# Kernel tuning notes

Measured on AMD Instinct MI355X. Metric: run time of the kernel, lower is better.

## Reference

```python
import jax, jax.numpy as jnp
import numpy as np

N, E, D, H, ED = 10000, 160000, 512, 256, 16
EPS = 1e-5  # BatchNorm1d eps


def _cgconv(x, src, dst, edge_attr, Wf, bf, Ws, bs, gamma, beta, mean, var):
    # PyG CGConv: z = [x_i, x_j, e_ij]; m = sigmoid(lin_f(z)) * softplus(lin_s(z));
    # aggr='add' at target i; batch_norm (eval mode, running stats) then residual.
    z = jnp.concatenate([x[dst], x[src], edge_attr], axis=1)  # [E, 2D+ED]
    m = jax.nn.sigmoid(z @ Wf + bf) * jax.nn.softplus(z @ Ws + bs)  # [E, D]
    aggr = jax.ops.segment_sum(m, dst, num_segments=x.shape[0])  # [N, D]
    bn = (aggr - mean) * jax.lax.rsqrt(var + EPS) * gamma + beta
    return x + bn


def _gcnconv(x, src, dst, W, b):
    # PyG GCNConv with add_self_loops=True, normalize=True:
    n = x.shape[0]
    deg = jax.ops.segment_sum(jnp.ones((src.shape[0],), x.dtype), dst, num_segments=n) + 1.0
    dinv = jax.lax.rsqrt(deg)  # [N]
    h = x @ W  # [N, out]
    out = jax.ops.segment_sum((dinv[src] * dinv[dst])[:, None] * h[src], dst, num_segments=n)
    out = out + (dinv * dinv)[:, None] * h  # self-loop contribution
    return out + b


def _forward(x, edge_attr, goal_feat,
             cg1_Wf, cg1_bf, cg1_Ws, cg1_bs, cg1_gamma, cg1_beta, cg1_mean, cg1_var,
             cg2_Wf, cg2_bf, cg2_Ws, cg2_bs, cg2_gamma, cg2_beta, cg2_mean, cg2_var,
             gcn3_W, gcn3_b, gcn4_W, gcn4_b, d1_W, d1_b, d2_W, d2_b, src, dst):
    # dropout layers are identity in eval mode (self.training=False)
    x = jax.nn.relu(_cgconv(x, src, dst, edge_attr, cg1_Wf, cg1_bf, cg1_Ws, cg1_bs,
                            cg1_gamma, cg1_beta, cg1_mean, cg1_var))
    x = jax.nn.relu(_cgconv(x, src, dst, edge_attr, cg2_Wf, cg2_bf, cg2_Ws, cg2_bs,
                            cg2_gamma, cg2_beta, cg2_mean, cg2_var))
    x = jax.nn.relu(_gcnconv(x, src, dst, gcn3_W, gcn3_b))
    x = jax.nn.relu(_gcnconv(x, src, dst, gcn4_W, gcn4_b))
    g = jnp.broadcast_to(goal_feat, (x.shape[0], goal_feat.shape[1]))  # repeat(num_nodes, 1)
    h = jax.nn.relu(jnp.concatenate([x, g], axis=1) @ d1_W + d1_b)
    return h @ d2_W + d2_b  # [N, 1]


def setup_inputs() -> dict:
    ks = jax.random.split(jax.random.key(0), 12)
    w = lambda k, s: jax.random.normal(k, s, dtype=jnp.float32) * 0.02
    Z = 2 * D + ED
    return {
        "x": jax.random.normal(ks[0], (N, D), jnp.float32),
        "edge_attr": jax.random.normal(ks[1], (E, ED), jnp.float32),
        "goal_feat": jax.random.normal(ks[2], (1, D), jnp.float32),
        "cg1_Wf": w(ks[3], (Z, D)), "cg1_bf": jnp.zeros((D,), jnp.float32),
        "cg1_Ws": w(ks[4], (Z, D)), "cg1_bs": jnp.zeros((D,), jnp.float32),
        "cg1_gamma": jnp.ones((D,), jnp.float32), "cg1_beta": jnp.zeros((D,), jnp.float32),
        "cg1_mean": jnp.zeros((D,), jnp.float32), "cg1_var": jnp.ones((D,), jnp.float32),
        "cg2_Wf": w(ks[5], (Z, D)), "cg2_bf": jnp.zeros((D,), jnp.float32),
        "cg2_Ws": w(ks[6], (Z, D)), "cg2_bs": jnp.zeros((D,), jnp.float32),
        "cg2_gamma": jnp.ones((D,), jnp.float32), "cg2_beta": jnp.zeros((D,), jnp.float32),
        "cg2_mean": jnp.zeros((D,), jnp.float32), "cg2_var": jnp.ones((D,), jnp.float32),
        "gcn3_W": w(ks[7], (D, H)), "gcn3_b": jnp.zeros((H,), jnp.float32),
        "gcn4_W": w(ks[8], (H, H)), "gcn4_b": jnp.zeros((H,), jnp.float32),
        "d1_W": w(ks[9], (H + D, D)), "d1_b": jnp.zeros((D,), jnp.float32),
        "d2_W": w(ks[10], (D, 1)), "d2_b": jnp.zeros((1,), jnp.float32),
        "edge_index": jax.random.randint(ks[11], (2, E), 0, N, dtype=jnp.int32),
        "batch": jnp.zeros((N,), jnp.int32),
    }


def reference(x, edge_attr, goal_feat,
              cg1_Wf, cg1_bf, cg1_Ws, cg1_bs, cg1_gamma, cg1_beta, cg1_mean, cg1_var,
              cg2_Wf, cg2_bf, cg2_Ws, cg2_bs, cg2_gamma, cg2_beta, cg2_mean, cg2_var,
              gcn3_W, gcn3_b, gcn4_W, gcn4_b, d1_W, d1_b, d2_W, d2_b,
              edge_index, batch):
    src, dst = edge_index[0], edge_index[1]
    return _forward(x, edge_attr, goal_feat,
                    cg1_Wf, cg1_bf, cg1_Ws, cg1_bs, cg1_gamma, cg1_beta, cg1_mean, cg1_var,
                    cg2_Wf, cg2_bf, cg2_Ws, cg2_bs, cg2_gamma, cg2_beta, cg2_mean, cg2_var,
                    gcn3_W, gcn3_b, gcn4_W, gcn4_b, d1_W, d1_b, d2_W, d2_b, src, dst)
```

## Files before the change

### kernel.cpp

```cpp
#include <hip/hip_runtime.h>
#include <math.h>

#define N_NODES 10000
#define N_EDGES 160000
#define DIM 512
#define HDIM 256
#define EDIM 16
#define BN_EPS 1e-5f
#define L2E 1.4426950408889634f
#define LN2 0.6931471805599453f

typedef unsigned short ushort_t;
typedef unsigned int uint_t;
typedef __attribute__((ext_vector_type(8))) short bf16x8;
typedef __attribute__((ext_vector_type(4))) float f32x4;
typedef __attribute__((ext_vector_type(2))) _Float16 half2_t;

__device__ __forceinline__ ushort_t f2bf(float x) {
    uint_t u = __float_as_uint(x);
    uint_t r = (u + 0x7FFF + ((u >> 16) & 1)) >> 16;
    return (ushort_t)r;
}
__device__ __forceinline__ float bf2f(ushort_t h) {
    return __uint_as_float(((uint_t)h) << 16);
}
__device__ __forceinline__ float bflo(uint_t u) {
    return __uint_as_float(u << 16);
}
__device__ __forceinline__ float bfhi(uint_t u) {
    return __uint_as_float(u & 0xffff0000u);
}
__device__ __forceinline__ void gld16(const void* g, void* l) {
    __builtin_amdgcn_global_load_lds(
        (const __attribute__((address_space(1))) unsigned int*)g,
        (__attribute__((address_space(3))) unsigned int*)l, 16, 0, 0);
}
__device__ __forceinline__ half2_t u2h(uint_t u) {
    return __builtin_bit_cast(half2_t, u);
}
__device__ __forceinline__ uint_t pk_f16(float a, float b) {
    return __builtin_bit_cast(uint_t, __builtin_amdgcn_cvt_pkrtz(a, b));
}
__device__ __forceinline__ float fexp2(float x) {
#if __has_builtin(__builtin_amdgcn_exp2f)
    return __builtin_amdgcn_exp2f(x);
#else
    return __expf(x * LN2);
#endif
}
__device__ __forceinline__ float flog2(float x) {
#if __has_builtin(__builtin_amdgcn_logf)
    return __builtin_amdgcn_logf(x);
#else
    return __logf(x) * L2E;
#endif
}
__device__ __forceinline__ void swz(int lid, int gx, int gy, int& bx, int& by) {
    int per = gy * 8;
    int grp = lid / per;
    int rem = lid - grp * per;
    int gsz = min(8, gx - grp * 8);
    by = rem / gsz;
    bx = grp * 8 + (rem - by * gsz);
}

__global__ void k_hist(const int* __restrict__ dst, int* __restrict__ cnt) {
    int e = blockIdx.x * blockDim.x + threadIdx.x;
    if (e < N_EDGES) atomicAdd(&cnt[dst[e]], 1);
}

__global__ __launch_bounds__(1024) void k_scan(int* __restrict__ offs, float* __restrict__ dinv) {
    __shared__ int wsum[16];
    __shared__ int carryS;
    int t = threadIdx.x, lane = t & 63, wv = t >> 6;
    if (t == 0) carryS = 0;
    __syncthreads();
    for (int base = 0; base < N_NODES; base += 1024) {
        int idx = base + t;
        int v = (idx < N_NODES) ? offs[idx] : 0;
        if (idx < N_NODES) dinv[idx] = rsqrtf((float)v + 1.0f);
        int s = v;
#pragma unroll
        for (int off = 1; off < 64; off <<= 1) {
            int u = __shfl_up(s, off, 64);
            if (lane >= off) s += u;
        }
        if (lane == 63) wsum[wv] = s;
        __syncthreads();
        int carry = carryS;
        if (wv == 0) {
            int w = (lane < 16) ? wsum[lane] : 0;
#pragma unroll
            for (int off = 1; off < 16; off <<= 1) {
                int u = __shfl_up(w, off, 64);
                if (lane >= off) w += u;
            }
            if (lane < 16) wsum[lane] = w;
        }
        __syncthreads();
        int wbase = (wv == 0) ? 0 : wsum[wv - 1];
        if (idx < N_NODES) offs[idx] = carry + wbase + s - v;
        int total = wsum[15];
        __syncthreads();
        if (t == 0) carryS = carry + total;
        __syncthreads();
    }
    if (t == 0) offs[N_NODES] = carryS;
}

__global__ void k_scatter(const int* __restrict__ srcv, const int* __restrict__ dstv,
                          const float* __restrict__ ea,
                          const int* __restrict__ offs, const float* __restrict__ dinv,
                          int* __restrict__ cursor,
                          int* __restrict__ srcArr, float* __restrict__ dinvArr,
                          uint_t* __restrict__ eaP) {
    int e = blockIdx.x * blockDim.x + threadIdx.x;
    if (e >= N_EDGES) return;
    int d = dstv[e];
    int p = offs[d] + atomicAdd(&cursor[d], 1);
    int s = srcv[e];
    srcArr[p] = s;
    dinvArr[p] = dinv[s];
    const float* er = ea + (size_t)e * EDIM;
    uint_t pk[8];
#pragma unroll
    for (int k2 = 0; k2 < 8; k2++) pk[k2] = pk_f16(er[2 * k2], er[2 * k2 + 1]);
    uint_t* q = eaP + (size_t)p * 8;
    *(uint4*)q = *(uint4*)&pk[0];
    *(uint4*)(q + 4) = *(uint4*)&pk[4];
}

__global__ __launch_bounds__(256) void k_cvtW(
    const float* __restrict__ Wf0, const float* __restrict__ Ws0,
    const float* __restrict__ Wf1, const float* __restrict__ Ws1,
    const float* __restrict__ g3W, const float* __restrict__ g4W,
    const float* __restrict__ d1W,
    ushort_t* __restrict__ W2cg0, ushort_t* __restrict__ W2cg1,
    ushort_t* __restrict__ W2g3, ushort_t* __restrict__ W2g4,
    ushort_t* __restrict__ W2d1)
{
    __shared__ ushort_t tle[64][72];
    int b = blockIdx.x, t = threadIdx.x;
    const float* src; int ldw, kin0, cin0, ldk, cout0, kout0; ushort_t* out; float scale;
    if (b < 512) {
        int layer = b >> 8, tt = b & 255;
        int g = tt >> 6, rem = tt & 63;
        int ct = rem >> 3, kt = rem & 7;
        const float* Wf = layer ? Wf1 : Wf0;
        const float* Ws = layer ? Ws1 : Ws0;
        src = (g & 1) ? Ws : Wf;
        ldw = 512; kin0 = ((g & 2) ? 512 : 0) + kt * 64; cin0 = ct * 64;
        out = layer ? W2cg1 : W2cg0; ldk = 512;
        cout0 = g * 512 + ct * 64; kout0 = kt * 64;
        scale = L2E;
    } else if (b < 544) {
        int tt = b - 512; int ct = tt >> 3, kt = tt & 7;
        src = g3W; ldw = 256; kin0 = kt * 64; cin0 = ct * 64;
        out = W2g3; ldk = 512; cout0 = ct * 64; kout0 = kt * 64; scale = 1.f;
    } else if (b < 560) {
        int tt = b - 544; int ct = tt >> 2, kt = tt & 3;
        src = g4W; ldw = 256; kin0 = kt * 64; cin0 = ct * 64;
        out = W2g4; ldk = 256; cout0 = ct * 64; kout0 = kt * 64; scale = 1.f;
    } else {
        int tt = b - 560; int ct = tt >> 2, kt = tt & 3;
        src = d1W; ldw = 512; kin0 = kt * 64; cin0 = ct * 64;
        out = W2d1; ldk = 256; cout0 = ct * 64; kout0 = kt * 64; scale = 1.f;
    }
    int c = t & 63;
    int k4 = t >> 6;
#pragma unroll
    for (int i = 0; i < 16; i++) {
        int k = k4 * 16 + i;
        tle[k][c] = f2bf(src[(size_t)(kin0 + k) * ldw + cin0 + c] * scale);
    }
    __syncthreads();
    int cl = t >> 2, kq = t & 3;
    ushort_t tmp[16];
#pragma unroll
    for (int j = 0; j < 16; j++) tmp[j] = tle[kq * 16 + j][cl];
    ushort_t* dst = out + (size_t)(cout0 + cl) * ldk + kout0 + kq * 16;
    *(uint4*)dst = *(uint4*)&tmp[0];
    *(uint4*)(dst + 8) = *(uint4*)&tmp[8];
}

#define MP_WEP   32
#define MP_GV    40
#define MP_END   20040

__global__ __launch_bounds__(256) void k_megaprep(
    const float* __restrict__ x, const float* __restrict__ goal,
    const float* __restrict__ Wf0, const float* __restrict__ Ws0,
    const float* __restrict__ Wf1, const float* __restrict__ Ws1,
    const float* __restrict__ d1W, const float* __restrict__ d1b,
    ushort_t* __restrict__ A2, uint_t* __restrict__ WEP, float* __restrict__ cgv)
{
    int b = blockIdx.x, t = threadIdx.x;
    if (b < MP_WEP) {
        int layer = b >> 4, blk = b & 15;
        int idx = blk * 256 + t;
        int c = idx >> 3, k2 = idx & 7;
        const float* Wf = (layer ? Wf1 : Wf0) + 1024 * 512;
        const float* Ws = (layer ? Ws1 : Ws0) + 1024 * 512;
        uint_t* WEPf = WEP + layer * 8192;
        uint_t* WEPs = WEPf + 4096;
        WEPf[c * 8 + k2] = pk_f16(Wf[(2 * k2) * 512 + c] * L2E, Wf[(2 * k2 + 1) * 512 + c] * L2E);
        WEPs[c * 8 + k2] = pk_f16(Ws[(2 * k2) * 512 + c] * L2E, Ws[(2 * k2 + 1) * 512 + c] * L2E);
    } else if (b < MP_GV) {
        __shared__ float red[256];
        int bb = b - MP_WEP;
        int c = bb * 64 + (t & 63);
        int slice = t >> 6;
        float acc = 0.f;
        for (int i = 0; i < 128; i++) {
            int k = slice * 128 + i;
            acc += goal[k] * d1W[(size_t)(256 + k) * 512 + c];
        }
        red[t] = acc;
        __syncthreads();
        if (t < 128) red[t] += red[t + 128];
        __syncthreads();
        if (t < 64) cgv[c] = red[t] + red[t + 64] + d1b[c];
    } else {
        int idx = (b - MP_GV) * 256 + t;
        if (idx < N_NODES * 512) A2[idx] = f2bf(x[idx]);
    }
}

__global__ __launch_bounds__(256) void k_gemm3(
    const ushort_t* __restrict__ A2, int K, int M,
    const ushort_t* __restrict__ W2t,
    float* __restrict__ outF, ushort_t* __restrict__ outQ,
    const float* __restrict__ bias, int mode, int ldc, int gx, int gy)
{
    __shared__ ushort_t As[128 * 64];
    __shared__ ushort_t Bs[128 * 64];
    int tid = threadIdx.x;
    int lane = tid & 63, w = tid >> 6;
    int wm = w & 1, wn = w >> 1;
    int lrow = lane & 15, quad = lane >> 4;
    int bx, by;
    swz(blockIdx.x, gx, gy, bx, by);
    int row0 = bx * 128, col0 = by * 128;

    f32x4 acc[4][4] = {};

    const ushort_t* ArG[4]; ushort_t* ArL[4];
    const ushort_t* BrG[4]; ushort_t* BrL[4];
#pragma unroll
    for (int p = 0; p < 4; p++) {
        int s = tid + 256 * p;
        int r = s >> 3, k8p = s & 7;
        int k8l = k8p ^ (r & 7);
        int gra = row0 + r; if (gra >= M) gra = M - 1;
        ArG[p] = A2 + (size_t)gra * K + k8l * 8;
        ArL[p] = As + s * 8;
        BrG[p] = W2t + (size_t)(col0 + r) * K + k8l * 8;
        BrL[p] = Bs + s * 8;
    }
    const ushort_t* afp[2][4];
    const ushort_t* bfp[2][4];
#pragma unroll
    for (int sl = 0; sl < 2; sl++)
#pragma unroll
        for (int mt = 0; mt < 4; mt++) {
            int r = wm * 64 + mt * 16 + lrow;
            afp[sl][mt] = As + (r * 8 + ((sl * 4 + quad) ^ (r & 7))) * 8;
            int c = wn * 64 + mt * 16 + lrow;
            bfp[sl][mt] = Bs + (c * 8 + ((sl * 4 + quad) ^ (c & 7))) * 8;
        }

    for (int k0 = 0; k0 < K; k0 += 64) {
        __syncthreads();
#pragma unroll
        for (int p = 0; p < 4; p++) {
            gld16(ArG[p] + k0, ArL[p]);
            gld16(BrG[p] + k0, BrL[p]);
        }
        __syncthreads();
#pragma unroll
        for (int sl = 0; sl < 2; sl++) {
            bf16x8 af[4], bff[4];
#pragma unroll
            for (int i = 0; i < 4; i++) {
                af[i]  = *(const bf16x8*)afp[sl][i];
                bff[i] = *(const bf16x8*)bfp[sl][i];
            }
#pragma unroll
            for (int mt = 0; mt < 4; mt++)
#pragma unroll
                for (int nt = 0; nt < 4; nt++)
                    acc[mt][nt] = __builtin_amdgcn_mfma_f32_16x16x32_bf16(
                        af[mt], bff[nt], acc[mt][nt], 0, 0, 0);
        }
    }

#pragma unroll
    for (int mt = 0; mt < 4; mt++) {
#pragma unroll
        for (int nt = 0; nt < 4; nt++) {
            int gcol = col0 + wn * 64 + nt * 16 + lrow;
#pragma unroll
            for (int r = 0; r < 4; r++) {
                int grow = row0 + wm * 64 + mt * 16 + quad * 4 + r;
                if (grow >= M) continue;
                float v = acc[mt][nt][r];
                if (mode == 1) {
                    if (gcol < 1024) {
                        outF[(size_t)grow * 1024 + gcol] = v;
                    } else {
                        int c = gcol - 1024;
                        int grp = c >> 9, cc = c & 511;
                        int pos = (cc >> 1) * 4 + grp * 2 + (cc & 1);
                        outQ[(size_t)grow * 1024 + pos] = f2bf(v);
                    }
                } else if (mode == 2) {
                    outF[(size_t)grow * ldc + gcol] = fmaxf(v + bias[gcol], 0.f);
                } else {
                    outQ[(size_t)grow * ldc + gcol] = f2bf(v);
                }
            }
        }
    }
}

__global__ __launch_bounds__(256) void k_gemm64(
    const ushort_t* __restrict__ A2, int K, int M,
    const ushort_t* __restrict__ W2t,
    float* __restrict__ outF, ushort_t* __restrict__ outQ,
    const float* __restrict__ bias, int mode, int ldc, int gx, int gy)
{
    __shared__ ushort_t As[64 * 64];
    __shared__ ushort_t Bs[128 * 64];
    int tid = threadIdx.x;
    int lane = tid & 63, w = tid >> 6;
    int lrow = lane & 15, quad = lane >> 4;
    int bx, by;
    swz(blockIdx.x, gx, gy, bx, by);
    int row0 = bx * 64, col0 = by * 128;

    f32x4 acc[4][2] = {};

    const ushort_t* ArG[2]; ushort_t* ArL[2];
    const ushort_t* BrG[4]; ushort_t* BrL[4];
#pragma unroll
    for (int p = 0; p < 2; p++) {
        int s = tid + 256 * p;
        int r = s >> 3, k8p = s & 7;
        int k8l = k8p ^ (r & 7);
        int gra = row0 + r; if (gra >= M) gra = M - 1;
        ArG[p] = A2 + (size_t)gra * K + k8l * 8;
        ArL[p] = As + s * 8;
    }
#pragma unroll
    for (int p = 0; p < 4; p++) {
        int s = tid + 256 * p;
        int r = s >> 3, k8p = s & 7;
        int k8l = k8p ^ (r & 7);
        BrG[p] = W2t + (size_t)(col0 + r) * K + k8l * 8;
        BrL[p] = Bs + s * 8;
    }
    const ushort_t* afp[2][4];
    const ushort_t* bfp[2][2];
#pragma unroll
    for (int sl = 0; sl < 2; sl++) {
#pragma unroll
        for (int mt = 0; mt < 4; mt++) {
            int r = mt * 16 + lrow;
            afp[sl][mt] = As + (r * 8 + ((sl * 4 + quad) ^ (r & 7))) * 8;
        }
#pragma unroll
        for (int nt = 0; nt < 2; nt++) {
            int c = w * 32 + nt * 16 + lrow;
            bfp[sl][nt] = Bs + (c * 8 + ((sl * 4 + quad) ^ (c & 7))) * 8;
        }
    }

    for (int k0 = 0; k0 < K; k0 += 64) {
        __syncthreads();
        gld16(ArG[0] + k0, ArL[0]);
        gld16(ArG[1] + k0, ArL[1]);
#pragma unroll
        for (int p = 0; p < 4; p++) gld16(BrG[p] + k0, BrL[p]);
        __syncthreads();
#pragma unroll
        for (int sl = 0; sl < 2; sl++) {
            bf16x8 af[4], bff[2];
#pragma unroll
            for (int i = 0; i < 4; i++) af[i] = *(const bf16x8*)afp[sl][i];
#pragma unroll
            for (int i = 0; i < 2; i++) bff[i] = *(const bf16x8*)bfp[sl][i];
#pragma unroll
            for (int mt = 0; mt < 4; mt++)
#pragma unroll
                for (int nt = 0; nt < 2; nt++)
                    acc[mt][nt] = __builtin_amdgcn_mfma_f32_16x16x32_bf16(
                        af[mt], bff[nt], acc[mt][nt], 0, 0, 0);
        }
    }

#pragma unroll
    for (int mt = 0; mt < 4; mt++) {
#pragma unroll
        for (int nt = 0; nt < 2; nt++) {
            int gcol = col0 + w * 32 + nt * 16 + lrow;
#pragma unroll
            for (int r = 0; r < 4; r++) {
                int grow = row0 + mt * 16 + quad * 4 + r;
                if (grow >= M) continue;
                float v = acc[mt][nt][r];
                if (mode == 2) outF[(size_t)grow * ldc + gcol] = fmaxf(v + bias[gcol], 0.f);
                else outQ[(size_t)grow * ldc + gcol] = f2bf(v);
            }
        }
    }
}

__global__ __launch_bounds__(256) void k_cg_aggr(
    const float* __restrict__ xin, const float* __restrict__ P,
    const ushort_t* __restrict__ Qi,
    const uint_t* __restrict__ WEPf, const uint_t* __restrict__ WEPs,
    const float* __restrict__ bfv, const float* __restrict__ bsv,
    const float* __restrict__ gamma, const float* __restrict__ beta,
    const float* __restrict__ mean, const float* __restrict__ var,
    const int* __restrict__ offs, const int* __restrict__ srcArr,
    const uint_t* __restrict__ eaP,
    float* __restrict__ xout, ushort_t* __restrict__ A2out)
{
    int i = blockIdx.x;
    int t = threadIdx.x;
    int c0 = 2 * t;
    uint_t wfp[2][8], wsp[2][8];
    {
        const uint_t* pf8 = WEPf + c0 * 8;
        const uint_t* ps8 = WEPs + c0 * 8;
        *(uint4*)&wfp[0][0] = *(const uint4*)(pf8 + 0);
        *(uint4*)&wfp[0][4] = *(const uint4*)(pf8 + 4);
        *(uint4*)&wfp[1][0] = *(const uint4*)(pf8 + 8);
        *(uint4*)&wfp[1][4] = *(const uint4*)(pf8 + 12);
        *(uint4*)&wsp[0][0] = *(const uint4*)(ps8 + 0);
        *(uint4*)&wsp[0][4] = *(const uint4*)(ps8 + 4);
        *(uint4*)&wsp[1][0] = *(const uint4*)(ps8 + 8);
        *(uint4*)&wsp[1][4] = *(const uint4*)(ps8 + 12);
    }
    float2 pf = *(const float2*)&P[(size_t)i * 1024 + c0];
    float2 ps = *(const float2*)&P[(size_t)i * 1024 + 512 + c0];
    float2 bf2 = *(const float2*)&bfv[c0];
    float2 bs2 = *(const float2*)&bsv[c0];
    pf.x = fmaf(bf2.x, L2E, pf.x); pf.y = fmaf(bf2.y, L2E, pf.y);
    ps.x = fmaf(bs2.x, L2E, ps.x); ps.y = fmaf(bs2.y, L2E, ps.y);
    float acc0 = 0.f, acc1 = 0.f;
    int e0 = offs[i], e1 = offs[i + 1];
    __shared__ uint_t sEaP[32][8];
    __shared__ int sSrc[34];
    const ushort_t* Qbase = Qi + 4 * t;
    for (int base = e0; base < e1; base += 32) {
        int g = min(32, e1 - base);
        __syncthreads();
        if (t < 34) {
            int s = 0;
            if (t < g) s = srcArr[base + t];
            sSrc[t] = s;
        }
        {
            int j = t >> 3, k2 = t & 7;
            if (j < g) sEaP[j][k2] = eaP[(size_t)(base + j) * 8 + k2];
        }
        __syncthreads();
        uint2 q0 = *(const uint2*)(Qbase + ((size_t)sSrc[0] << 10));
        uint2 q1 = *(const uint2*)(Qbase + ((size_t)sSrc[1] << 10));
        for (int j = 0; j < g; j++) {
            uint2 qn = *(const uint2*)(Qbase + ((size_t)sSrc[j + 2] << 10));
            uint4 eA = *(const uint4*)&sEaP[j][0];
            uint4 eB = *(const uint4*)&sEaP[j][4];
            float gf0 = pf.x + bflo(q0.x), gf1 = pf.y + bfhi(q0.x);
            float gs0 = ps.x + bflo(q0.y), gs1 = ps.y + bfhi(q0.y);
            uint_t ek[8] = {eA.x, eA.y, eA.z, eA.w, eB.x, eB.y, eB.z, eB.w};
#pragma unroll
            for (int k = 0; k < 8; k++) {
                half2_t e2 = u2h(ek[k]);
                gf0 = __builtin_amdgcn_fdot2(e2, u2h(wfp[0][k]), gf0, false);
                gf1 = __builtin_amdgcn_fdot2(e2, u2h(wfp[1][k]), gf1, false);
                gs0 = __builtin_amdgcn_fdot2(e2, u2h(wsp[0][k]), gs0, false);
                gs1 = __builtin_amdgcn_fdot2(e2, u2h(wsp[1][k]), gs1, false);
            }
            float sg0 = __builtin_amdgcn_rcpf(1.f + fexp2(-gf0));
            float sg1 = __builtin_amdgcn_rcpf(1.f + fexp2(-gf1));
            float sp0 = fmaxf(gs0, 0.f) + flog2(1.f + fexp2(-fabsf(gs0)));
            float sp1 = fmaxf(gs1, 0.f) + flog2(1.f + fexp2(-fabsf(gs1)));
            acc0 = fmaf(sg0, sp0, acc0);
            acc1 = fmaf(sg1, sp1, acc1);
            q0 = q1; q1 = qn;
        }
    }
    acc0 *= LN2;
    acc1 *= LN2;
    size_t ib = (size_t)i * DIM;
    float2 mn = *(const float2*)&mean[c0];
    float2 vr = *(const float2*)&var[c0];
    float2 gm = *(const float2*)&gamma[c0];
    float2 bt = *(const float2*)&beta[c0];
    float2 xi = *(const float2*)&xin[ib + c0];
    float bn0 = (acc0 - mn.x) * rsqrtf(vr.x + BN_EPS) * gm.x + bt.x;
    float bn1 = (acc1 - mn.y) * rsqrtf(vr.y + BN_EPS) * gm.y + bt.y;
    float o0 = fmaxf(xi.x + bn0, 0.f);
    float o1 = fmaxf(xi.y + bn1, 0.f);
    if (xout) *(float2*)&xout[ib + c0] = make_float2(o0, o1);
    ushort_t h0 = f2bf(o0), h1 = f2bf(o1);
    *(uint_t*)(A2out + (size_t)i * 512 + c0) = (uint_t)h0 | ((uint_t)h1 << 16);
}

__global__ __launch_bounds__(128) void k_gcn_aggr(
    const ushort_t* __restrict__ h, const float* __restrict__ dinv,
    const float* __restrict__ bias,
    const int* __restrict__ offs, const int* __restrict__ srcArr,
    const float* __restrict__ dinvArr, ushort_t* __restrict__ A2out)
{
    int i = blockIdx.x;
    int t = threadIdx.x;
    int c0 = 2 * t;
    float acc0 = 0.f, acc1 = 0.f;
    int e0 = offs[i], e1 = offs[i + 1];
    __shared__ int sS[36];
    __shared__ float sD[36];
    for (int base = e0; base < e1; base += 32) {
        int g = min(32, e1 - base);
        __syncthreads();
        if (t < 36) {
            bool ok = (t < g);
            sS[t] = ok ? srcArr[base + t] : 0;
            sD[t] = ok ? dinvArr[base + t] : 0.f;
        }
        __syncthreads();
        uint_t q0 = *(const uint_t*)(h + (size_t)sS[0] * HDIM + c0);
        uint_t q1 = *(const uint_t*)(h + (size_t)sS[1] * HDIM + c0);
        uint_t q2 = *(const uint_t*)(h + (size_t)sS[2] * HDIM + c0);
        uint_t q3 = *(const uint_t*)(h + (size_t)sS[3] * HDIM + c0);
        for (int j = 0; j < g; j++) {
            uint_t qn = *(const uint_t*)(h + (size_t)sS[j + 4] * HDIM + c0);
            acc0 += sD[j] * bflo(q0);
            acc1 += sD[j] * bfhi(q0);
            q0 = q1; q1 = q2; q2 = q3; q3 = qn;
        }
    }
    float di = dinv[i];
    uint_t qi = *(const uint_t*)(h + (size_t)i * HDIM + c0);
    float2 b2 = *(const float2*)&bias[c0];
    float o0 = fmaxf(di * acc0 + di * di * bflo(qi) + b2.x, 0.f);
    float o1 = fmaxf(di * acc1 + di * di * bfhi(qi) + b2.y, 0.f);
    ushort_t h0 = f2bf(o0), h1 = f2bf(o1);
    *(uint_t*)(A2out + (size_t)i * 256 + c0) = (uint_t)h0 | ((uint_t)h1 << 16);
}

__global__ __launch_bounds__(256) void k_final(const float* __restrict__ hd,
                                               const float* __restrict__ w2,
                                               const float* __restrict__ b2,
                                               float* __restrict__ out) {
    int wave = threadIdx.x >> 6, lane = threadIdx.x & 63;
    int i = blockIdx.x * 4 + wave;
    if (i >= N_NODES) return;
    const float* r = hd + (size_t)i * DIM;
    float acc = 0.f;
#pragma unroll
    for (int q = 0; q < 8; q++) acc += r[lane + 64 * q] * w2[lane + 64 * q];
#pragma unroll
    for (int off = 32; off > 0; off >>= 1) acc += __shfl_down(acc, off, 64);
    if (lane == 0) out[i] = acc + b2[0];
}

extern "C" void kernel_launch(void* const* d_in, const int* in_sizes, int n_in,
                              void* d_out, int out_size, void* d_ws, size_t ws_size,
                              hipStream_t stream) {
    (void)in_sizes; (void)n_in; (void)out_size; (void)ws_size;
    const float* x      = (const float*)d_in[0];
    const float* ea     = (const float*)d_in[1];
    const float* goal   = (const float*)d_in[2];
    const float* cgWf[2] = {(const float*)d_in[3],  (const float*)d_in[11]};
    const float* cgbf[2] = {(const float*)d_in[4],  (const float*)d_in[12]};
    const float* cgWs[2] = {(const float*)d_in[5],  (const float*)d_in[13]};
    const float* cgbs[2] = {(const float*)d_in[6],  (const float*)d_in[14]};
    const float* cggm[2] = {(const float*)d_in[7],  (const float*)d_in[15]};
    const float* cgbt[2] = {(const float*)d_in[8],  (const float*)d_in[16]};
    const float* cgmn[2] = {(const float*)d_in[9],  (const float*)d_in[17]};
    const float* cgvr[2] = {(const float*)d_in[10], (const float*)d_in[18]};
    const float* gcn3_W = (const float*)d_in[19];
    const float* gcn3_b = (const float*)d_in[20];
    const float* gcn4_W = (const float*)d_in[21];
    const float* gcn4_b = (const float*)d_in[22];
    const float* d1_W   = (const float*)d_in[23];
    const float* d1_b   = (const float*)d_in[24];
    const float* d2_W   = (const float*)d_in[25];
    const float* d2_b   = (const float*)d_in[26];
    const int*   eidx   = (const int*)d_in[27];
    const int*   srcv   = eidx;
    const int*   dstv   = eidx + N_EDGES;
    float* outp = (float*)d_out;

    char* w = (char*)d_ws;
    float*    Pbuf  = (float*)w;                      w += (size_t)N_NODES * 1024 * 4;
    ushort_t* Qbuf  = (ushort_t*)w;                   w += (size_t)N_NODES * 1024 * 2;
    float*    xB    = (float*)w;                      w += (size_t)N_NODES * 512 * 4;
    ushort_t* A2    = (ushort_t*)w;                   w += (size_t)N_NODES * 512 * 2;
    ushort_t* A3    = (ushort_t*)w;                   w += (size_t)N_NODES * 256 * 2;
    ushort_t* W2cg0 = (ushort_t*)w;                   w += (size_t)2048 * 512 * 2;
    ushort_t* W2cg1 = (ushort_t*)w;                   w += (size_t)2048 * 512 * 2;
    ushort_t* W2g3  = (ushort_t*)w;                   w += (size_t)256 * 512 * 2;
    ushort_t* W2g4  = (ushort_t*)w;                   w += (size_t)256 * 256 * 2;
    ushort_t* W2d1  = (ushort_t*)w;                   w += (size_t)512 * 256 * 2;
    uint_t*   eaP   = (uint_t*)w;                     w += (size_t)N_EDGES * 8 * 4;
    uint_t*   WEP   = (uint_t*)w;                     w += 16384 * 4;
    float*    cgv   = (float*)w;                      w += 512 * 4;
    int*      srcArr  = (int*)w;                      w += N_EDGES * 4;
    float*    dinvArr = (float*)w;                    w += N_EDGES * 4;
    int*      offs    = (int*)w;                      w += (N_NODES + 1) * 4;
    int*      cursor  = (int*)w;                      w += N_NODES * 4;
    float*    dinv    = (float*)w;                    w += N_NODES * 4;
    uint_t* WEPf[2] = {WEP, WEP + 8192};
    uint_t* WEPs[2] = {WEP + 4096, WEP + 12288};
    ushort_t* h3 = (ushort_t*)Pbuf;
    float*    hd = (float*)Qbuf;

    k_cvtW<<<592, 256, 0, stream>>>(cgWf[0], cgWs[0], cgWf[1], cgWs[1],
                                    gcn3_W, gcn4_W, d1_W,
                                    W2cg0, W2cg1, W2g3, W2g4, W2d1);
    k_megaprep<<<MP_END, 256, 0, stream>>>(x, goal,
        cgWf[0], cgWs[0], cgWf[1], cgWs[1], d1_W, d1_b, A2, WEP, cgv);

    hipMemsetAsync(offs, 0, (N_NODES + 1) * sizeof(int), stream);
    hipMemsetAsync(cursor, 0, N_NODES * sizeof(int), stream);
    k_hist<<<(N_EDGES + 255) / 256, 256, 0, stream>>>(dstv, offs);
    k_scan<<<1, 1024, 0, stream>>>(offs, dinv);
    k_scatter<<<(N_EDGES + 255) / 256, 256, 0, stream>>>(srcv, dstv, ea, offs, dinv,
                                                         cursor, srcArr, dinvArr, eaP);

    k_gemm3<<<79 * 16, 256, 0, stream>>>(A2, 512, N_NODES, W2cg0,
                                         Pbuf, Qbuf, nullptr, 1, 0, 79, 16);
    k_cg_aggr<<<N_NODES, 256, 0, stream>>>(x, Pbuf, Qbuf, WEPf[0], WEPs[0],
                                           cgbf[0], cgbs[0],
                                           cggm[0], cgbt[0], cgmn[0], cgvr[0],
                                           offs, srcArr, eaP, xB, A2);
    k_gemm3<<<79 * 16, 256, 0, stream>>>(A2, 512, N_NODES, W2cg1,
                                         Pbuf, Qbuf, nullptr, 1, 0, 79, 16);
    k_cg_aggr<<<N_NODES, 256, 0, stream>>>(xB, Pbuf, Qbuf, WEPf[1], WEPs[1],
                                           cgbf[1], cgbs[1],
                                           cggm[1], cgbt[1], cgmn[1], cgvr[1],
                                           offs, srcArr, eaP, nullptr, A2);

    k_gemm64<<<157 * 2, 256, 0, stream>>>(A2, 512, N_NODES, W2g3,
                                          nullptr, h3, nullptr, 3, HDIM, 157, 2);
    k_gcn_aggr<<<N_NODES, 128, 0, stream>>>(h3, dinv, gcn3_b, offs, srcArr, dinvArr, A3);

    k_gemm64<<<157 * 2, 256, 0, stream>>>(A3, 256, N_NODES, W2g4,
                                          nullptr, h3, nullptr, 3, HDIM, 157, 2);
    k_gcn_aggr<<<N_NODES, 128, 0, stream>>>(h3, dinv, gcn4_b, offs, srcArr, dinvArr, A3);

    k_gemm64<<<157 * 4, 256, 0, stream>>>(A3, 256, N_NODES, W2d1,
                                          hd, nullptr, cgv, 2, DIM, 157, 4);
    k_final<<<(N_NODES + 3) / 4, 256, 0, stream>>>(hd, d2_W, d2_b, outp);
}
```

Before: 561.4 us.

## Deepen gather prefetch in aggregation kernels and single-pass scan

The CG and GCN aggregation loops now prefetch 4 and 8 neighbor rows ahead using a rotating register ring, with the loop unrolled to match. The scatter kernel stores source indices already scaled to byte offsets, so the gathers skip the multiply. The CSR scan becomes a single pass where each thread handles 10 nodes, replacing the serial loop over 1024-node chunks. The aim is more memory-level parallelism on the random gathers and less scan latency. The cost is extra register pressure and a second index array to write.

Measured after the change: 536.0 us. 1.05x faster.

```diff
diff --git a/kernel.cpp b/kernel.cpp
--- a/kernel.cpp
+++ b/kernel.cpp
@@ -71,55 +71,61 @@
 
 __global__ __launch_bounds__(1024) void k_scan(int* __restrict__ offs, float* __restrict__ dinv) {
     __shared__ int wsum[16];
-    __shared__ int carryS;
     int t = threadIdx.x, lane = t & 63, wv = t >> 6;
-    if (t == 0) carryS = 0;
+    int base_i = t * 10;
+    int v[10];
+    int s = 0;
+#pragma unroll
+    for (int k = 0; k < 10; k++) {
+        int idx = base_i + k;
+        int x = (idx < N_NODES) ? offs[idx] : 0;
+        v[k] = x;
+        s += x;
+        if (idx < N_NODES) dinv[idx] = rsqrtf((float)x + 1.0f);
+    }
+    int ps = s;
+#pragma unroll
+    for (int off = 1; off < 64; off <<= 1) {
+        int u = __shfl_up(ps, off, 64);
+        if (lane >= off) ps += u;
+    }
+    if (lane == 63) wsum[wv] = ps;
     __syncthreads();
-    for (int base = 0; base < N_NODES; base += 1024) {
-        int idx = base + t;
-        int v = (idx < N_NODES) ? offs[idx] : 0;
-        if (idx < N_NODES) dinv[idx] = rsqrtf((float)v + 1.0f);
-        int s = v;
-#pragma unroll
-        for (int off = 1; off < 64; off <<= 1) {
-            int u = __shfl_up(s, off, 64);
-            if (lane >= off) s += u;
-        }
-        if (lane == 63) wsum[wv] = s;
-        __syncthreads();
-        int carry = carryS;
-        if (wv == 0) {
-            int w = (lane < 16) ? wsum[lane] : 0;
-#pragma unroll
-            for (int off = 1; off < 16; off <<= 1) {
-                int u = __shfl_up(w, off, 64);
-                if (lane >= off) w += u;
-            }
-            if (lane < 16) wsum[lane] = w;
-        }
-        __syncthreads();
-        int wbase = (wv == 0) ? 0 : wsum[wv - 1];
-        if (idx < N_NODES) offs[idx] = carry + wbase + s - v;
-        int total = wsum[15];
-        __syncthreads();
-        if (t == 0) carryS = carry + total;
-        __syncthreads();
-    }
-    if (t == 0) offs[N_NODES] = carryS;
+    if (wv == 0) {
+        int w = (lane < 16) ? wsum[lane] : 0;
+#pragma unroll
+        for (int off = 1; off < 16; off <<= 1) {
+            int u = __shfl_up(w, off, 64);
+            if (lane >= off) w += u;
+        }
+        if (lane < 16) wsum[lane] = w;
+    }
+    __syncthreads();
+    int wbase = (wv == 0) ? 0 : wsum[wv - 1];
+    int run = wbase + ps - s;
+#pragma unroll
+    for (int k = 0; k < 10; k++) {
+        int idx = base_i + k;
+        if (idx < N_NODES) offs[idx] = run;
+        run += v[k];
+    }
+    if (t == 1023) offs[N_NODES] = wsum[15];
 }
 
 __global__ void k_scatter(const int* __restrict__ srcv, const int* __restrict__ dstv,
                           const float* __restrict__ ea,
                           const int* __restrict__ offs, const float* __restrict__ dinv,
                           int* __restrict__ cursor,
-                          int* __restrict__ srcArr, float* __restrict__ dinvArr,
+                          int* __restrict__ srcQ, int* __restrict__ srcH,
+                          float* __restrict__ dinvArr,
                           uint_t* __restrict__ eaP) {
     int e = blockIdx.x * blockDim.x + threadIdx.x;
     if (e >= N_EDGES) return;
     int d = dstv[e];
     int p = offs[d] + atomicAdd(&cursor[d], 1);
     int s = srcv[e];
-    srcArr[p] = s;
+    srcQ[p] = s << 11;
+    srcH[p] = s << 9;
     dinvArr[p] = dinv[s];
     const float* er = ea + (size_t)e * EDIM;
     uint_t pk[8];
@@ -415,6 +421,28 @@
     }
 }
 
+#define CG_BODY(curq, jj) do {                                                     \
+    uint4 eA = *(const uint4*)&sEaP[jj][0];                                        \
+    uint4 eB = *(const uint4*)&sEaP[jj][4];                                        \
+    float gf0 = pf.x + bflo((curq).x), gf1 = pf.y + bfhi((curq).x);                \
+    float gs0 = ps.x + bflo((curq).y), gs1 = ps.y + bfhi((curq).y);                \
+    uint_t ek[8] = {eA.x, eA.y, eA.z, eA.w, eB.x, eB.y, eB.z, eB.w};               \
+    _Pragma("unroll")                                                              \
+    for (int k = 0; k < 8; k++) {                                                  \
+        half2_t e2 = u2h(ek[k]);                                                   \
+        gf0 = __builtin_amdgcn_fdot2(e2, u2h(wfp[0][k]), gf0, false);              \
+        gf1 = __builtin_amdgcn_fdot2(e2, u2h(wfp[1][k]), gf1, false);              \
+        gs0 = __builtin_amdgcn_fdot2(e2, u2h(wsp[0][k]), gs0, false);              \
+        gs1 = __builtin_amdgcn_fdot2(e2, u2h(wsp[1][k]), gs1, false);              \
+    }                                                                              \
+    float sg0 = __builtin_amdgcn_rcpf(1.f + fexp2(-gf0));                          \
+    float sg1 = __builtin_amdgcn_rcpf(1.f + fexp2(-gf1));                          \
+    float sp0 = fmaxf(gs0, 0.f) + flog2(1.f + fexp2(-fabsf(gs0)));                 \
+    float sp1 = fmaxf(gs1, 0.f) + flog2(1.f + fexp2(-fabsf(gs1)));                 \
+    acc0 = fmaf(sg0, sp0, acc0);                                                   \
+    acc1 = fmaf(sg1, sp1, acc1);                                                   \
+} while (0)
+
 __global__ __launch_bounds__(256) void k_cg_aggr(
     const float* __restrict__ xin, const float* __restrict__ P,
     const ushort_t* __restrict__ Qi,
@@ -422,7 +450,7 @@
     const float* __restrict__ bfv, const float* __restrict__ bsv,
     const float* __restrict__ gamma, const float* __restrict__ beta,
     const float* __restrict__ mean, const float* __restrict__ var,
-    const int* __restrict__ offs, const int* __restrict__ srcArr,
+    const int* __restrict__ offs, const int* __restrict__ srcQ,
     const uint_t* __restrict__ eaP,
     float* __restrict__ xout, ushort_t* __restrict__ A2out)
 {
@@ -451,45 +479,32 @@
     float acc0 = 0.f, acc1 = 0.f;
     int e0 = offs[i], e1 = offs[i + 1];
     __shared__ uint_t sEaP[32][8];
-    __shared__ int sSrc[34];
-    const ushort_t* Qbase = Qi + 4 * t;
+    __shared__ int sOff[36];
+    const char* Qb = (const char*)(Qi + 4 * t);
     for (int base = e0; base < e1; base += 32) {
         int g = min(32, e1 - base);
         __syncthreads();
-        if (t < 34) {
-            int s = 0;
-            if (t < g) s = srcArr[base + t];
-            sSrc[t] = s;
-        }
+        if (t < 36) sOff[t] = (t < g) ? srcQ[base + t] : 0;
         {
             int j = t >> 3, k2 = t & 7;
             if (j < g) sEaP[j][k2] = eaP[(size_t)(base + j) * 8 + k2];
         }
         __syncthreads();
-        uint2 q0 = *(const uint2*)(Qbase + ((size_t)sSrc[0] << 10));
-        uint2 q1 = *(const uint2*)(Qbase + ((size_t)sSrc[1] << 10));
-        for (int j = 0; j < g; j++) {
-            uint2 qn = *(const uint2*)(Qbase + ((size_t)sSrc[j + 2] << 10));
-            uint4 eA = *(const uint4*)&sEaP[j][0];
-            uint4 eB = *(const uint4*)&sEaP[j][4];
-            float gf0 = pf.x + bflo(q0.x), gf1 = pf.y + bfhi(q0.x);
-            float gs0 = ps.x + bflo(q0.y), gs1 = ps.y + bfhi(q0.y);
-            uint_t ek[8] = {eA.x, eA.y, eA.z, eA.w, eB.x, eB.y, eB.z, eB.w};
-#pragma unroll
-            for (int k = 0; k < 8; k++) {
-                half2_t e2 = u2h(ek[k]);
-                gf0 = __builtin_amdgcn_fdot2(e2, u2h(wfp[0][k]), gf0, false);
-                gf1 = __builtin_amdgcn_fdot2(e2, u2h(wfp[1][k]), gf1, false);
-                gs0 = __builtin_amdgcn_fdot2(e2, u2h(wsp[0][k]), gs0, false);
-                gs1 = __builtin_amdgcn_fdot2(e2, u2h(wsp[1][k]), gs1, false);
+        uint2 q[4];
+#pragma unroll
+        for (int p = 0; p < 4; p++) q[p] = *(const uint2*)(Qb + (uint_t)sOff[p]);
+        int j = 0;
+        for (; j + 4 <= g; j += 4) {
+#pragma unroll
+            for (int u = 0; u < 4; u++) {
+                uint2 cur = q[u];
+                q[u] = *(const uint2*)(Qb + (uint_t)sOff[j + u + 4]);
+                CG_BODY(cur, j + u);
             }
-            float sg0 = __builtin_amdgcn_rcpf(1.f + fexp2(-gf0));
-            float sg1 = __builtin_amdgcn_rcpf(1.f + fexp2(-gf1));
-            float sp0 = fmaxf(gs0, 0.f) + flog2(1.f + fexp2(-fabsf(gs0)));
-            float sp1 = fmaxf(gs1, 0.f) + flog2(1.f + fexp2(-fabsf(gs1)));
-            acc0 = fmaf(sg0, sp0, acc0);
-            acc1 = fmaf(sg1, sp1, acc1);
-            q0 = q1; q1 = qn;
+        }
+#pragma unroll
+        for (int u = 0; u < 3; u++) {
+            if (j + u < g) CG_BODY(q[u], j + u);
         }
     }
     acc0 *= LN2;
@@ -512,7 +527,7 @@
 __global__ __launch_bounds__(128) void k_gcn_aggr(
     const ushort_t* __restrict__ h, const float* __restrict__ dinv,
     const float* __restrict__ bias,
-    const int* __restrict__ offs, const int* __restrict__ srcArr,
+    const int* __restrict__ offs, const int* __restrict__ srcH,
     const float* __restrict__ dinvArr, ushort_t* __restrict__ A2out)
 {
     int i = blockIdx.x;
@@ -520,26 +535,40 @@
     int c0 = 2 * t;
     float acc0 = 0.f, acc1 = 0.f;
     int e0 = offs[i], e1 = offs[i + 1];
-    __shared__ int sS[36];
-    __shared__ float sD[36];
+    __shared__ int sS[40];
+    __shared__ float sD[40];
+    const char* hb = (const char*)(h + c0);
     for (int base = e0; base < e1; base += 32) {
         int g = min(32, e1 - base);
         __syncthreads();
-        if (t < 36) {
+        if (t < 40) {
             bool ok = (t < g);
-            sS[t] = ok ? srcArr[base + t] : 0;
+            sS[t] = ok ? srcH[base + t] : 0;
             sD[t] = ok ? dinvArr[base + t] : 0.f;
         }
         __syncthreads();
-        uint_t q0 = *(const uint_t*)(h + (size_t)sS[0] * HDIM + c0);
-        uint_t q1 = *(const uint_t*)(h + (size_t)sS[1] * HDIM + c0);
-        uint_t q2 = *(const uint_t*)(h + (size_t)sS[2] * HDIM + c0);
-        uint_t q3 = *(const uint_t*)(h + (size_t)sS[3] * HDIM + c0);
-        for (int j = 0; j < g; j++) {
-            uint_t qn = *(const uint_t*)(h + (size_t)sS[j + 4] * HDIM + c0);
-            acc0 += sD[j] * bflo(q0);
-            acc1 += sD[j] * bfhi(q0);
-            q0 = q1; q1 = q2; q2 = q3; q3 = qn;
+        uint_t q[8];
+#pragma unroll
+        for (int p = 0; p < 8; p++) q[p] = *(const uint_t*)(hb + (uint_t)sS[p]);
+        int j = 0;
+        for (; j + 8 <= g; j += 8) {
+#pragma unroll
+            for (int u = 0; u < 8; u++) {
+                uint_t cur = q[u];
+                q[u] = *(const uint_t*)(hb + (uint_t)sS[j + u + 8]);
+                float d = sD[j + u];
+                acc0 = fmaf(d, bflo(cur), acc0);
+                acc1 = fmaf(d, bfhi(cur), acc1);
+            }
+        }
+#pragma unroll
+        for (int u = 0; u < 7; u++) {
+            if (j + u < g) {
+                uint_t cur = q[u];
+                float d = sD[j + u];
+                acc0 = fmaf(d, bflo(cur), acc0);
+                acc1 = fmaf(d, bfhi(cur), acc1);
+            }
         }
     }
     float di = dinv[i];
@@ -609,7 +638,8 @@
     uint_t*   eaP   = (uint_t*)w;                     w += (size_t)N_EDGES * 8 * 4;
     uint_t*   WEP   = (uint_t*)w;                     w += 16384 * 4;
     float*    cgv   = (float*)w;                      w += 512 * 4;
-    int*      srcArr  = (int*)w;                      w += N_EDGES * 4;
+    int*      srcQ    = (int*)w;                      w += N_EDGES * 4;
+    int*      srcH    = (int*)w;                      w += N_EDGES * 4;
     float*    dinvArr = (float*)w;                    w += N_EDGES * 4;
     int*      offs    = (int*)w;                      w += (N_NODES + 1) * 4;
     int*      cursor  = (int*)w;                      w += N_NODES * 4;
@@ -630,28 +660,28 @@
     k_hist<<<(N_EDGES + 255) / 256, 256, 0, stream>>>(dstv, offs);
     k_scan<<<1, 1024, 0, stream>>>(offs, dinv);
     k_scatter<<<(N_EDGES + 255) / 256, 256, 0, stream>>>(srcv, dstv, ea, offs, dinv,
-                                                         cursor, srcArr, dinvArr, eaP);
+                                                         cursor, srcQ, srcH, dinvArr, eaP);
 
     k_gemm3<<<79 * 16, 256, 0, stream>>>(A2, 512, N_NODES, W2cg0,
                                          Pbuf, Qbuf, nullptr, 1, 0, 79, 16);
     k_cg_aggr<<<N_NODES, 256, 0, stream>>>(x, Pbuf, Qbuf, WEPf[0], WEPs[0],
                                            cgbf[0], cgbs[0],
                                            cggm[0], cgbt[0], cgmn[0], cgvr[0],
-                                           offs, srcArr, eaP, xB, A2);
+                                           offs, srcQ, eaP, xB, A2);
     k_gemm3<<<79 * 16, 256, 0, stream>>>(A2, 512, N_NODES, W2cg1,
                                          Pbuf, Qbuf, nullptr, 1, 0, 79, 16);
     k_cg_aggr<<<N_NODES, 256, 0, stream>>>(xB, Pbuf, Qbuf, WEPf[1], WEPs[1],
                                            cgbf[1], cgbs[1],
                                            cggm[1], cgbt[1], cgmn[1], cgvr[1],
-                                           offs, srcArr, eaP, nullptr, A2);
+                                           offs, srcQ, eaP, nullptr, A2);
 
     k_gemm64<<<157 * 2, 256, 0, stream>>>(A2, 512, N_NODES, W2g3,
                                           nullptr, h3, nullptr, 3, HDIM, 157, 2);
-    k_gcn_aggr<<<N_NODES, 128, 0, stream>>>(h3, dinv, gcn3_b, offs, srcArr, dinvArr, A3);
+    k_gcn_aggr<<<N_NODES, 128, 0, stream>>>(h3, dinv, gcn3_b, offs, srcH, dinvArr, A3);
 
     k_gemm64<<<157 * 2, 256, 0, stream>>>(A3, 256, N_NODES, W2g4,
                                           nullptr, h3, nullptr, 3, HDIM, 157, 2);
-    k_gcn_aggr<<<N_NODES, 128, 0, stream>>>(h3, dinv, gcn4_b, offs, srcArr, dinvArr, A3);
+    k_gcn_aggr<<<N_NODES, 128, 0, stream>>>(h3, dinv, gcn4_b, offs, srcH, dinvArr, A3);
 
     k_gemm64<<<157 * 4, 256, 0, stream>>>(A3, 256, N_NODES, W2d1,
                                           hd, nullptr, cgv, 2, DIM, 157, 4);
```
